# Performance work log

Measured on AMD Instinct MI355X. Metric: run time of the kernel, lower is better.

## Reference

```python
import jax, jax.numpy as jnp
import numpy as np

D_MODEL = 1024
NUM_EXPERTS = 16
TOP_K = 2
TOP_C = 4  # min(M, max(4, 2*K))
RANK = 64  # max(4, d_model // 16) per choose_lowrank_r
TAU = 1.0


def setup_inputs() -> dict:
    key = jax.random.key(0)
    ks = jax.random.split(key, 7)
    B = 32768
    x = jax.random.normal(ks[0], (B, D_MODEL), dtype=jnp.float32)
    # shared encoder Linear(d, d) with bias
    We = jax.random.normal(ks[1], (D_MODEL, D_MODEL), dtype=jnp.float32) / np.sqrt(D_MODEL)
    be = jnp.zeros((D_MODEL,), dtype=jnp.float32)
    # gating Linear(d, M), no bias
    Wg = jax.random.normal(ks[2], (NUM_EXPERTS, D_MODEL), dtype=jnp.float32) / np.sqrt(D_MODEL)
    # per-expert LoRA weights: U: [M, r, d], V: [M, d, r], gamma: [M]
    U = jax.random.normal(ks[3], (NUM_EXPERTS, RANK, D_MODEL), dtype=jnp.float32) / np.sqrt(D_MODEL)
    V = jax.random.normal(ks[4], (NUM_EXPERTS, D_MODEL, RANK), dtype=jnp.float32) / np.sqrt(RANK)
    gamma = jnp.ones((NUM_EXPERTS,), dtype=jnp.float32)
    return {"x": x, "We": We, "be": be, "Wg": Wg, "U": U, "V": V, "gamma": gamma}


def reference(x, We, be, Wg, U, V, gamma):
    B = x.shape[0]
    encoded = x @ We.T + be                       # [B, d]
    logits = (encoded @ Wg.T) / TAU               # [B, M]
    # Top-C candidate selection, then Top-K among candidates
    topc_vals, topc_idx = jax.lax.top_k(logits, TOP_C)          # [B, C]
    topk_vals, pos_in_c = jax.lax.top_k(topc_vals, TOP_K)       # [B, K]
    topk_idx = jnp.take_along_axis(topc_idx, pos_in_c, axis=1)  # [B, K]
    # masked stable softmax over selected logits (matches _stable_masked_softmax)
    e = jnp.exp(topk_vals - jnp.max(topk_vals, axis=1, keepdims=True))
    w = e / (jnp.sum(e, axis=1, keepdims=True) + 1e-12)
    w = jnp.where(w > 1e-12, w, 0.0)  # keep_mask: drop negligible weights
    # scatter routing weights into dense [B, M] combine matrix
    w_full = jnp.zeros((B, NUM_EXPERTS), x.dtype).at[
        jnp.arange(B)[:, None], topk_idx].add(w)
    # expert residual delta: E(x) = x + gamma * V @ silu(U @ x)
    hidden = jax.nn.silu(jnp.einsum('bd,mrd->bmr', encoded, U))  # [B, M, r]
    delta = jnp.einsum('bmr,mdr,bm->bd', hidden, V, w_full * gamma[None, :])
    # y = encoded + sum_k w_k * (E_k(encoded) - encoded); sum_k w_k = 1
    return encoded + delta
```

## Files before the change

### kernel.cpp

```cpp
#include <hip/hip_runtime.h>
#include <stdint.h>

#define B_TOK 32768
#define DM 1024
#define NEXP 16
#define RK 64
#define NPAIR 256
#define TPT 64
#define HT 128
#define GRID_CMB 3072
#define GRID_HID 544
#define MAXTILE 1024

typedef unsigned short u16;
typedef __bf16 bf16x8 __attribute__((ext_vector_type(8)));
typedef float f32x4 __attribute__((ext_vector_type(4)));

__device__ __forceinline__ u16 f2bf(float f) {
  union { float f; uint32_t u; } v; v.f = f;
  return (u16)((v.u + 0x7fffu + ((v.u >> 16) & 1u)) >> 16);
}
__device__ __forceinline__ float bf2f(u16 u) {
  union { uint32_t i; float f; } v; v.i = ((uint32_t)u) << 16; return v.f;
}

__device__ __forceinline__ void gload_lds16(const void* g, void* l) {
  __builtin_amdgcn_global_load_lds(
      (const __attribute__((address_space(1))) void*)g,
      (__attribute__((address_space(3))) void*)l, 16, 0, 0);
}

__global__ void k_convert(const float* __restrict__ src, u16* __restrict__ dst, int n4) {
  int i = blockIdx.x * blockDim.x + threadIdx.x;
  int stride = gridDim.x * blockDim.x;
  for (; i < n4; i += stride) {
    float4 v = reinterpret_cast<const float4*>(src)[i];
    ushort4 o;
    o.x = f2bf(v.x); o.y = f2bf(v.y); o.z = f2bf(v.z); o.w = f2bf(v.w);
    reinterpret_cast<ushort4*>(dst)[i] = o;
  }
}

__global__ void k_wgeff(const float* __restrict__ Wg, const float* __restrict__ We,
                        const float* __restrict__ be,
                        float* __restrict__ Wgeff, float* __restrict__ gbias) {
  int e = blockIdx.y;
  int d = blockIdx.x * 256 + threadIdx.x;
  double acc = 0.0;
  for (int k = 0; k < DM; ++k)
    acc += (double)Wg[e * DM + k] * (double)We[k * DM + d];
  Wgeff[e * DM + d] = (float)acc;
  if (blockIdx.x == 0 && threadIdx.x == 0) {
    double s = 0.0;
    for (int k = 0; k < DM; ++k) s += (double)be[k] * (double)Wg[e * DM + k];
    gbias[e] = (float)s;
  }
}

#define GT 64
#define GD 128

__global__ __launch_bounds__(256) void k_gating(
    const float* __restrict__ x, u16* __restrict__ x_bf,
    const float* __restrict__ Wgeff, const float* __restrict__ gbias,
    const float* __restrict__ gamma,
    int* __restrict__ tk_pid, float* __restrict__ tk_w0, float* __restrict__ tk_w1,
    int* __restrict__ counts_p, int* __restrict__ counts_e) {
  __shared__ float xs[GT][GD + 4];
  __shared__ float wsd[NEXP][GD + 4];
  __shared__ float lg[GT][NEXP + 2];
  __shared__ int bcnt[NPAIR];
  __shared__ int bexp[NEXP];
  const int tid = threadIdx.x;
  const int tok0 = blockIdx.x * GT;
  const int t0 = (tid >> 3) * 2;
  const int e0 = (tid & 7) * 2;
  bcnt[tid] = 0;
  if (tid < NEXP) bexp[tid] = 0;

  double acc00 = 0.0, acc01 = 0.0, acc10 = 0.0, acc11 = 0.0;

  for (int c = 0; c < DM; c += GD) {
    __syncthreads();
    #pragma unroll
    for (int v = 0; v < (GT * GD / 4) / 256; ++v) {
      int idx = tid + v * 256;
      int r = idx >> 5, cc = idx & 31;
      float4 v4 = *reinterpret_cast<const float4*>(x + (size_t)(tok0 + r) * DM + c + cc * 4);
      *reinterpret_cast<float4*>(&xs[r][cc * 4]) = v4;
      ushort4 o;
      o.x = f2bf(v4.x); o.y = f2bf(v4.y); o.z = f2bf(v4.z); o.w = f2bf(v4.w);
      *reinterpret_cast<ushort4*>(x_bf + (size_t)(tok0 + r) * DM + c + cc * 4) = o;
    }
    #pragma unroll
    for (int v = 0; v < (NEXP * GD / 4) / 256; ++v) {
      int idx = tid + v * 256;
      int r = idx >> 5, cc = idx & 31;
      *reinterpret_cast<float4*>(&wsd[r][cc * 4]) =
          *reinterpret_cast<const float4*>(Wgeff + (size_t)r * DM + c + cc * 4);
    }
    __syncthreads();
    #pragma unroll 8
    for (int d = 0; d < GD; d += 4) {
      float4 xa = *reinterpret_cast<const float4*>(&xs[t0][d]);
      float4 xb = *reinterpret_cast<const float4*>(&xs[t0 + 1][d]);
      float4 wa = *reinterpret_cast<const float4*>(&wsd[e0][d]);
      float4 wb = *reinterpret_cast<const float4*>(&wsd[e0 + 1][d]);
      acc00 += (double)xa.x * wa.x + (double)xa.y * wa.y + (double)xa.z * wa.z + (double)xa.w * wa.w;
      acc01 += (double)xa.x * wb.x + (double)xa.y * wb.y + (double)xa.z * wb.z + (double)xa.w * wb.w;
      acc10 += (double)xb.x * wa.x + (double)xb.y * wa.y + (double)xb.z * wa.z + (double)xb.w * wa.w;
      acc11 += (double)xb.x * wb.x + (double)xb.y * wb.y + (double)xb.z * wb.z + (double)xb.w * wb.w;
    }
  }

  lg[t0][e0]         = (float)(acc00 + (double)gbias[e0]);
  lg[t0][e0 + 1]     = (float)(acc01 + (double)gbias[e0 + 1]);
  lg[t0 + 1][e0]     = (float)(acc10 + (double)gbias[e0]);
  lg[t0 + 1][e0 + 1] = (float)(acc11 + (double)gbias[e0 + 1]);
  __syncthreads();

  if (tid < GT) {
    int tok = tok0 + tid;
    float v0 = lg[tid][0]; int i0 = 0;
    #pragma unroll
    for (int j = 1; j < NEXP; ++j)
      if (lg[tid][j] > v0) { v0 = lg[tid][j]; i0 = j; }
    float v1 = -3.4e38f; int i1 = 0;
    #pragma unroll
    for (int j = 0; j < NEXP; ++j) {
      if (j == i0) continue;
      if (lg[tid][j] > v1) { v1 = lg[tid][j]; i1 = j; }
    }
    float e1 = expf(v1 - v0);
    float denom = 1.0f + e1 + 1e-12f;
    float w0 = 1.0f / denom, w1 = e1 / denom;
    if (!(w0 > 1e-12f)) w0 = 0.0f;
    if (!(w1 > 1e-12f)) w1 = 0.0f;
    int pid = i0 * 16 + i1;
    tk_pid[tok] = pid;
    tk_w0[tok] = w0 * gamma[i0];
    tk_w1[tok] = w1 * gamma[i1];
    atomicAdd(&bcnt[pid], 1);
    atomicAdd(&bexp[i0], 1);
    atomicAdd(&bexp[i1], 1);
  }
  __syncthreads();
  if (bcnt[tid] > 0) atomicAdd(&counts_p[tid], bcnt[tid]);
  if (tid < NEXP && bexp[tid] > 0) atomicAdd(&counts_e[tid], bexp[tid]);
}

__global__ __launch_bounds__(NPAIR) void k_scan(
    const int* __restrict__ counts_p, const int* __restrict__ counts_e,
    int* __restrict__ offs_p, int* __restrict__ curs_p,
    int* __restrict__ offs_e, int* __restrict__ curs_e,
    int* __restrict__ tp_pair, int* __restrict__ tp_loc, int* __restrict__ n_tp,
    int* __restrict__ th_exp, int* __restrict__ th_loc, int* __restrict__ n_th) {
  __shared__ int sc[NPAIR], st[NPAIR];
  __shared__ int seb[NEXP + 1], thb[NEXP + 1];
  const int tid = threadIdx.x;
  const int c = counts_p[tid];
  const int nt = (c + TPT - 1) / TPT;
  sc[tid] = c; st[tid] = nt;
  __syncthreads();
  for (int s = 1; s < NPAIR; s <<= 1) {
    int vc = 0, vt = 0;
    if (tid >= s) { vc = sc[tid - s]; vt = st[tid - s]; }
    __syncthreads();
    sc[tid] += vc; st[tid] += vt;
    __syncthreads();
  }
  const int offc = sc[tid] - c;
  const int offt = st[tid] - nt;
  offs_p[tid] = offc;
  curs_p[tid] = offc;
  if (tid == NPAIR - 1) { offs_p[NPAIR] = sc[tid]; n_tp[0] = st[tid]; }
  for (int q = 0; q < nt; ++q) { tp_pair[offt + q] = tid; tp_loc[offt + q] = q * TPT; }

  if (tid == 0) {
    int s = 0, s2 = 0;
    for (int e = 0; e < NEXP; ++e) {
      seb[e] = s; thb[e] = s2;
      int ce = counts_e[e];
      s += ce; s2 += (ce + HT - 1) / HT;
    }
    seb[NEXP] = s; thb[NEXP] = s2;
    n_th[0] = s2;
  }
  __syncthreads();
  if (tid <= NEXP) offs_e[tid] = seb[tid];
  if (tid < NEXP) {
    curs_e[tid] = seb[tid];
    int ce = counts_e[tid];
    int ntt = (ce + HT - 1) / HT;
    for (int q = 0; q < ntt; ++q) { th_exp[thb[tid] + q] = tid; th_loc[thb[tid] + q] = q * HT; }
  }
}

__global__ __launch_bounds__(256) void k_scatter(
    const int* __restrict__ tk_pid, const float* __restrict__ tk_w0,
    const float* __restrict__ tk_w1,
    int* __restrict__ curs_p, int* __restrict__ curs_e,
    int* __restrict__ a_tok, int* __restrict__ a_h0,
    int* __restrict__ a_h1,
    int* __restrict__ e_tok, float* __restrict__ e_w) {
  __shared__ int hp[NPAIR];
  __shared__ int he[NEXP];
  __shared__ int bp[NPAIR];
  __shared__ int beB[NEXP];
  const int tid = threadIdx.x;
  const int tok = blockIdx.x * 256 + tid;
  hp[tid] = 0;
  if (tid < NEXP) he[tid] = 0;
  __syncthreads();

  const int pid = tk_pid[tok];
  const int i0 = pid >> 4, i1 = pid & 15;
  const int rp = atomicAdd(&hp[pid], 1);
  const int r0 = atomicAdd(&he[i0], 1);
  const int r1 = atomicAdd(&he[i1], 1);
  __syncthreads();

  if (hp[tid] > 0) bp[tid] = atomicAdd(&curs_p[tid], hp[tid]);
  if (tid < NEXP && he[tid] > 0) beB[tid] = atomicAdd(&curs_e[tid], he[tid]);
  __syncthreads();

  const int posp = bp[pid] + rp;
  const int pos0 = beB[i0] + r0;
  const int pos1 = beB[i1] + r1;
  a_tok[posp] = tok;
  a_h0[posp] = pos0;
  a_h1[posp] = pos1;
  e_tok[pos0] = tok; e_w[pos0] = tk_w0[tok];
  e_tok[pos1] = tok; e_w[pos1] = tk_w1[tok];
}

__global__ __launch_bounds__(256) void k_encoder(
    const u16* __restrict__ A, const u16* __restrict__ Bm,
    const float* __restrict__ bias, u16* __restrict__ Cb) {
  __shared__ __align__(16) u16 As[128 * 32];
  __shared__ __align__(16) u16 Bs[128 * 32];
  const int nwg = gridDim.x * gridDim.y;
  const int orig = blockIdx.y * gridDim.x + blockIdx.x;
  const int qq = nwg >> 3;
  const int swz = (orig & 7) * qq + (orig >> 3);
  const int m0 = (swz / gridDim.x) * 128, n0 = (swz % gridDim.x) * 128;
  const int tid = threadIdx.x;
  const int lane = tid & 63, wave = tid >> 6;
  const int wr = wave >> 1, wc = wave & 1;

  f32x4 acc[4][4];
  #pragma unroll
  for (int i = 0; i < 4; ++i)
    #pragma unroll
    for (int j = 0; j < 4; ++j) acc[i][j] = (f32x4){0.f, 0.f, 0.f, 0.f};

  const int srow = tid >> 2;
  const int scol = (tid & 3) * 8;
  const int lrow = lane & 15, lk = (lane >> 4) * 8;

  const u16* ga1 = A + (size_t)(m0 + srow) * DM + scol;
  const u16* ga2 = A + (size_t)(m0 + 64 + srow) * DM + scol;
  const u16* gb1 = Bm + (size_t)(n0 + srow) * DM + scol;
  const u16* gb2 = Bm + (size_t)(n0 + 64 + srow) * DM + scol;

  for (int k0 = 0; k0 < DM; k0 += 32) {
    __syncthreads();
    gload_lds16(ga1 + k0, As + srow * 32 + scol);
    gload_lds16(ga2 + k0, As + (64 + srow) * 32 + scol);
    gload_lds16(gb1 + k0, Bs + srow * 32 + scol);
    gload_lds16(gb2 + k0, Bs + (64 + srow) * 32 + scol);
    __syncthreads();
    bf16x8 a[4], b[4];
    #pragma unroll
    for (int mi = 0; mi < 4; ++mi)
      a[mi] = *reinterpret_cast<const bf16x8*>(&As[(wr * 64 + mi * 16 + lrow) * 32 + lk]);
    #pragma unroll
    for (int nj = 0; nj < 4; ++nj)
      b[nj] = *reinterpret_cast<const bf16x8*>(&Bs[(wc * 64 + nj * 16 + lrow) * 32 + lk]);
    #pragma unroll
    for (int mi = 0; mi < 4; ++mi)
      #pragma unroll
      for (int nj = 0; nj < 4; ++nj)
        acc[mi][nj] = __builtin_amdgcn_mfma_f32_16x16x32_bf16(a[mi], b[nj], acc[mi][nj], 0, 0, 0);
  }

  const int orow = (lane >> 4) * 4, ocol = lane & 15;
  #pragma unroll
  for (int mi = 0; mi < 4; ++mi) {
    #pragma unroll
    for (int nj = 0; nj < 4; ++nj) {
      int gcol = n0 + wc * 64 + nj * 16 + ocol;
      float bv = bias[gcol];
      #pragma unroll
      for (int r = 0; r < 4; ++r) {
        int grow = m0 + wr * 64 + mi * 16 + orow + r;
        Cb[(size_t)grow * DM + gcol] = f2bf(acc[mi][nj][r] + bv);
      }
    }
  }
}

__global__ __launch_bounds__(256) void k_hidden(
    const u16* __restrict__ Enc, const u16* __restrict__ Ub,
    const int* __restrict__ offs_e, const int* __restrict__ th_exp,
    const int* __restrict__ th_loc, const int* __restrict__ n_th,
    const int* __restrict__ e_tok, const float* __restrict__ e_w,
    u16* __restrict__ Hws) {
  const int bswz = (blockIdx.x & 7) * (GRID_HID >> 3) + (blockIdx.x >> 3);
  if (bswz >= n_th[0]) return;
  const int e = th_exp[bswz];
  const int loc0 = th_loc[bswz];
  const int base = offs_e[e];
  const int cnt = offs_e[e + 1] - base;
  const int tid = threadIdx.x;
  const int lane = tid & 63, wave = tid >> 6;
  const int lrow = lane & 15;
  const int lkb = (lane >> 4) * 16;

  __shared__ float s_ew[HT];
  __shared__ __align__(16) u16 Us[64 * 512];
  if (tid < HT) {
    int i = loc0 + tid;
    s_ew[tid] = (i < cnt) ? e_w[base + i] : 0.0f;
  }

  const u16* aP[2];
  #pragma unroll
  for (int mi = 0; mi < 2; ++mi) {
    int ridx = loc0 + wave * 32 + mi * 16 + lrow;
    int v = ridx < cnt;
    int tok = e_tok[base + (v ? ridx : 0)];
    aP[mi] = Enc + (size_t)tok * DM + (lane >> 4) * 8;
  }

  f32x4 acc[2][4];
  #pragma unroll
  for (int i = 0; i < 2; ++i)
    #pragma unroll
    for (int j = 0; j < 4; ++j) acc[i][j] = (f32x4){0.f, 0.f, 0.f, 0.f};

  const char* Ue = (const char*)(Ub + (size_t)e * RK * DM);

  for (int half = 0; half < 2; ++half) {
    __syncthreads();
    #pragma unroll
    for (int it = 0; it < 16; ++it) {
      int D = (tid + it * 256) * 16;
      int row = D >> 10, bo = D & 1023;
      int sbo = bo ^ ((row & 7) << 4);
      gload_lds16(Ue + (size_t)row * 2048 + half * 1024 + sbo, ((char*)Us) + D);
    }
    __syncthreads();
    #pragma unroll 4
    for (int step = 0; step < 16; ++step) {
      const int k0 = half * 512 + step * 32;
      bf16x8 b[4];
      #pragma unroll
      for (int nj = 0; nj < 4; ++nj) {
        int n = nj * 16 + lrow;
        int bofs = n * 1024 + ((step * 64 + lkb) ^ ((n & 7) << 4));
        b[nj] = *reinterpret_cast<const bf16x8*>(((const char*)Us) + bofs);
      }
      bf16x8 a0 = *reinterpret_cast<const bf16x8*>(aP[0] + k0);
      bf16x8 a1 = *reinterpret_cast<const bf16x8*>(aP[1] + k0);
      #pragma unroll
      for (int nj = 0; nj < 4; ++nj) {
        acc[0][nj] = __builtin_amdgcn_mfma_f32_16x16x32_bf16(a0, b[nj], acc[0][nj], 0, 0, 0);
        acc[1][nj] = __builtin_amdgcn_mfma_f32_16x16x32_bf16(a1, b[nj], acc[1][nj], 0, 0, 0);
      }
    }
  }

  #pragma unroll
  for (int mi = 0; mi < 2; ++mi)
    #pragma unroll
    for (int nj = 0; nj < 4; ++nj)
      #pragma unroll
      for (int rr = 0; rr < 4; ++rr) {
        int rloc = wave * 32 + mi * 16 + (lane >> 4) * 4 + rr;
        if (loc0 + rloc < cnt) {
          float z = acc[mi][nj][rr];
          float h = z / (1.0f + expf(-z)) * s_ew[rloc];
          Hws[(size_t)(base + loc0 + rloc) * RK + nj * 16 + (lane & 15)] = f2bf(h);
        }
      }
}

__global__ __launch_bounds__(256) void k_combine(
    const u16* __restrict__ Enc, const u16* __restrict__ Vb,
    const u16* __restrict__ Hws, const int* __restrict__ offs_p,
    const int* __restrict__ tp_pair, const int* __restrict__ tp_loc,
    const int* __restrict__ n_tp, const int* __restrict__ a_tok,
    const int* __restrict__ a_h0, const int* __restrict__ a_h1,
    float* __restrict__ Out) {
  const int bswz = (blockIdx.x & 7) * (GRID_CMB >> 3) + (blockIdx.x >> 3);
  const int t = bswz >> 2;
  const int p = bswz & 3;
  if (t >= n_tp[0]) return;
  const int pid = tp_pair[t];
  const int pe0 = pid >> 4, pe1 = pid & 15;
  const int base = offs_p[pid];
  const int cnt = offs_p[pid + 1] - base;
  const int loc0 = tp_loc[t];
  const int tid = threadIdx.x;
  const int lane = tid & 63, wave = tid >> 6;

  __shared__ int s_tok[TPT];
  __shared__ int s_h0[TPT];
  __shared__ int s_h1[TPT];
  __shared__ int s_val[TPT];
  if (tid < TPT) {
    int idx = loc0 + tid;
    int v = idx < cnt;
    int pp = base + (v ? idx : 0);
    s_val[tid] = v;
    s_tok[tid] = a_tok[pp];
    s_h0[tid] = a_h0[pp];
    s_h1[tid] = a_h1[pp];
  }
  __syncthreads();

  const int lrow = lane & 15, lk = (lane >> 4) * 8;

  bf16x8 hb[4][4];
  #pragma unroll
  for (int kk = 0; kk < 4; ++kk)
    #pragma unroll
    for (int tf = 0; tf < 4; ++tf) {
      int tok = tf * 16 + lrow;
      int hidx = (kk < 2) ? s_h0[tok] : s_h1[tok];
      hb[kk][tf] = *reinterpret_cast<const bf16x8*>(
          Hws + (size_t)hidx * RK + (kk & 1) * 32 + lk);
    }

  const u16* V0 = Vb + (size_t)pe0 * DM * RK;
  const u16* V1 = Vb + (size_t)pe1 * DM * RK;

  const int col0 = p * 256 + wave * 64;
  f32x4 acc2[4][4];
  #pragma unroll
  for (int i = 0; i < 4; ++i)
    #pragma unroll
    for (int j = 0; j < 4; ++j) acc2[i][j] = (f32x4){0.f, 0.f, 0.f, 0.f};

  #pragma unroll
  for (int kk = 0; kk < 4; ++kk) {
    const u16* Vsel = (kk < 2) ? V0 : V1;
    const int kof = (kk & 1) * 32 + lk;
    #pragma unroll
    for (int mi = 0; mi < 4; ++mi) {
      int d = col0 + mi * 16 + lrow;
      bf16x8 va = *reinterpret_cast<const bf16x8*>(Vsel + (size_t)d * RK + kof);
      #pragma unroll
      for (int tf = 0; tf < 4; ++tf)
        acc2[mi][tf] = __builtin_amdgcn_mfma_f32_16x16x32_bf16(va, hb[kk][tf], acc2[mi][tf], 0, 0, 0);
    }
  }

  #pragma unroll
  for (int mi = 0; mi < 4; ++mi)
    #pragma unroll
    for (int tf = 0; tf < 4; ++tf) {
      int tok = tf * 16 + (lane & 15);
      if (!s_val[tok]) continue;
      int d = col0 + mi * 16 + (lane >> 4) * 4;
      size_t ro = (size_t)s_tok[tok] * DM + d;
      ushort4 ev = *reinterpret_cast<const ushort4*>(Enc + ro);
      float4 o;
      o.x = acc2[mi][tf][0] + bf2f(ev.x);
      o.y = acc2[mi][tf][1] + bf2f(ev.y);
      o.z = acc2[mi][tf][2] + bf2f(ev.z);
      o.w = acc2[mi][tf][3] + bf2f(ev.w);
      *reinterpret_cast<float4*>(Out + ro) = o;
    }
}

extern "C" void kernel_launch(void* const* d_in, const int* in_sizes, int n_in,
                              void* d_out, int out_size, void* d_ws, size_t ws_size,
                              hipStream_t stream) {
  const float* x = (const float*)d_in[0];
  const float* We = (const float*)d_in[1];
  const float* be = (const float*)d_in[2];
  const float* Wg = (const float*)d_in[3];
  const float* U = (const float*)d_in[4];
  const float* V = (const float*)d_in[5];
  const float* gamma = (const float*)d_in[6];
  float* Out = (float*)d_out;

  char* ws = (char*)d_ws;
  size_t off = 0;
  auto alloc = [&](size_t bytes) -> void* {
    void* p = ws + off;
    off += (bytes + 255) & ~(size_t)255;
    return p;
  };
  u16* x_bf   = (u16*)alloc((size_t)B_TOK * DM * 2);
  u16* enc_bf = (u16*)alloc((size_t)B_TOK * DM * 2);
  u16* We_bf  = (u16*)alloc((size_t)DM * DM * 2);
  u16* U_bf   = (u16*)alloc((size_t)NEXP * RK * DM * 2);
  u16* V_bf   = (u16*)alloc((size_t)NEXP * DM * RK * 2);
  u16* Hws    = (u16*)alloc(((size_t)2 * B_TOK + HT) * RK * 2);
  float* Wgeff = (float*)alloc((size_t)NEXP * DM * 4);
  float* gbias = (float*)alloc(NEXP * 4);
  int* tk_pid  = (int*)alloc((size_t)B_TOK * 4);
  float* tk_w0 = (float*)alloc((size_t)B_TOK * 4);
  float* tk_w1 = (float*)alloc((size_t)B_TOK * 4);
  int* counts_p = (int*)alloc(NPAIR * 4);
  int* counts_e = (int*)alloc(NEXP * 4);
  int* offs_p   = (int*)alloc((NPAIR + 1) * 4);
  int* curs_p   = (int*)alloc(NPAIR * 4);
  int* offs_e   = (int*)alloc((NEXP + 1) * 4);
  int* curs_e   = (int*)alloc(NEXP * 4);
  int* tp_pair  = (int*)alloc(MAXTILE * 4);
  int* tp_loc   = (int*)alloc(MAXTILE * 4);
  int* n_tp     = (int*)alloc(256);
  int* th_exp   = (int*)alloc(MAXTILE * 4);
  int* th_loc   = (int*)alloc(MAXTILE * 4);
  int* n_th     = (int*)alloc(256);
  int* a_tok   = (int*)alloc((size_t)B_TOK * 4);
  int* a_h0    = (int*)alloc((size_t)B_TOK * 4);
  int* a_h1    = (int*)alloc((size_t)B_TOK * 4);
  int* e_tok   = (int*)alloc(((size_t)2 * B_TOK + HT) * 4);
  float* e_w   = (float*)alloc(((size_t)2 * B_TOK + HT) * 4);
  (void)ws_size; (void)in_sizes; (void)n_in; (void)out_size;

  hipMemsetAsync(counts_p, 0, NPAIR * 4, stream);
  hipMemsetAsync(counts_e, 0, NEXP * 4, stream);

  k_convert<<<256, 256, 0, stream>>>(We, We_bf, DM * DM / 4);
  k_convert<<<256, 256, 0, stream>>>(U, U_bf, NEXP * RK * DM / 4);
  k_convert<<<256, 256, 0, stream>>>(V, V_bf, NEXP * DM * RK / 4);
  k_wgeff<<<dim3(4, 16), 256, 0, stream>>>(Wg, We, be, Wgeff, gbias);
  k_gating<<<B_TOK / GT, 256, 0, stream>>>(x, x_bf, Wgeff, gbias, gamma,
                                           tk_pid, tk_w0, tk_w1, counts_p, counts_e);
  k_scan<<<1, NPAIR, 0, stream>>>(counts_p, counts_e, offs_p, curs_p, offs_e, curs_e,
                                  tp_pair, tp_loc, n_tp, th_exp, th_loc, n_th);
  k_scatter<<<B_TOK / 256, 256, 0, stream>>>(tk_pid, tk_w0, tk_w1, curs_p, curs_e,
                                             a_tok, a_h0, a_h1, e_tok, e_w);
  k_encoder<<<dim3(DM / 128, B_TOK / 128), 256, 0, stream>>>(x_bf, We_bf, be, enc_bf);
  k_hidden<<<GRID_HID, 256, 0, stream>>>(enc_bf, U_bf, offs_e, th_exp, th_loc, n_th,
                                         e_tok, e_w, Hws);
  k_combine<<<GRID_CMB, 256, 0, stream>>>(enc_bf, V_bf, Hws, offs_p, tp_pair, tp_loc,
                                          n_tp, a_tok, a_h0, a_h1, Out);
}
```

Measured before the change: 392.6 us.

## Widen encoder K-tile with XOR-swizzled LDS, stage epilogue, prefetch residual loads

The encoder GEMM now loads 64-wide K slices into LDS using an XOR swizzle to avoid bank conflicts, which halves the number of sync barriers per K loop. Its epilogue writes results to shared memory first and then stores them with coalesced 16-byte global writes instead of scattered 2-byte stores. In the combine kernel, the encoded residual values are loaded before the MFMA loop so their latency overlaps with the compute. These changes add register pressure from the prefetched residuals, and the shared-memory footprint grows to 32KB.

```diff
diff --git a/kernel.cpp b/kernel.cpp
--- a/kernel.cpp
+++ b/kernel.cpp
@@ -237,8 +237,9 @@
 __global__ __launch_bounds__(256) void k_encoder(
     const u16* __restrict__ A, const u16* __restrict__ Bm,
     const float* __restrict__ bias, u16* __restrict__ Cb) {
-  __shared__ __align__(16) u16 As[128 * 32];
-  __shared__ __align__(16) u16 Bs[128 * 32];
+  __shared__ __align__(16) u16 SM[128 * 128];
+  u16* As = SM;
+  u16* Bs = SM + 128 * 64;
   const int nwg = gridDim.x * gridDim.y;
   const int orig = blockIdx.y * gridDim.x + blockIdx.x;
   const int qq = nwg >> 3;
@@ -247,6 +248,7 @@
   const int tid = threadIdx.x;
   const int lane = tid & 63, wave = tid >> 6;
   const int wr = wave >> 1, wc = wave & 1;
+  const int lrow = lane & 15, lhi = lane >> 4;
 
   f32x4 acc[4][4];
   #pragma unroll
@@ -254,50 +256,61 @@
     #pragma unroll
     for (int j = 0; j < 4; ++j) acc[i][j] = (f32x4){0.f, 0.f, 0.f, 0.f};
 
-  const int srow = tid >> 2;
-  const int scol = (tid & 3) * 8;
-  const int lrow = lane & 15, lk = (lane >> 4) * 8;
-
-  const u16* ga1 = A + (size_t)(m0 + srow) * DM + scol;
-  const u16* ga2 = A + (size_t)(m0 + 64 + srow) * DM + scol;
-  const u16* gb1 = Bm + (size_t)(n0 + srow) * DM + scol;
-  const u16* gb2 = Bm + (size_t)(n0 + 64 + srow) * DM + scol;
-
-  for (int k0 = 0; k0 < DM; k0 += 32) {
-    __syncthreads();
-    gload_lds16(ga1 + k0, As + srow * 32 + scol);
-    gload_lds16(ga2 + k0, As + (64 + srow) * 32 + scol);
-    gload_lds16(gb1 + k0, Bs + srow * 32 + scol);
-    gload_lds16(gb2 + k0, Bs + (64 + srow) * 32 + scol);
-    __syncthreads();
-    bf16x8 a[4], b[4];
+  for (int k0 = 0; k0 < DM; k0 += 64) {
+    __syncthreads();
+    #pragma unroll
+    for (int j = 0; j < 4; ++j) {
+      int slot = wave * 256 + j * 64 + lane;
+      int r = slot >> 3, c = slot & 7;
+      int sc = (c ^ (r & 7)) << 3;
+      gload_lds16(A + (size_t)(m0 + r) * DM + k0 + sc, As + slot * 8);
+      gload_lds16(Bm + (size_t)(n0 + r) * DM + k0 + sc, Bs + slot * 8);
+    }
+    __syncthreads();
+    #pragma unroll
+    for (int kk = 0; kk < 2; ++kk) {
+      bf16x8 a[4], b[4];
+      #pragma unroll
+      for (int mi = 0; mi < 4; ++mi) {
+        int r = wr * 64 + mi * 16 + lrow;
+        a[mi] = *reinterpret_cast<const bf16x8*>(
+            As + r * 64 + ((((kk << 2) + lhi) ^ (r & 7)) << 3));
+      }
+      #pragma unroll
+      for (int nj = 0; nj < 4; ++nj) {
+        int r = wc * 64 + nj * 16 + lrow;
+        b[nj] = *reinterpret_cast<const bf16x8*>(
+            Bs + r * 64 + ((((kk << 2) + lhi) ^ (r & 7)) << 3));
+      }
+      #pragma unroll
+      for (int mi = 0; mi < 4; ++mi)
+        #pragma unroll
+        for (int nj = 0; nj < 4; ++nj)
+          acc[mi][nj] = __builtin_amdgcn_mfma_f32_16x16x32_bf16(a[mi], b[nj], acc[mi][nj], 0, 0, 0);
+    }
+  }
+
+  __syncthreads();
+  const int orow = lhi * 4, ocol = lrow;
+  #pragma unroll
+  for (int nj = 0; nj < 4; ++nj) {
+    int col_l = wc * 64 + nj * 16 + ocol;
+    float bv = bias[n0 + col_l];
     #pragma unroll
     for (int mi = 0; mi < 4; ++mi)
-      a[mi] = *reinterpret_cast<const bf16x8*>(&As[(wr * 64 + mi * 16 + lrow) * 32 + lk]);
-    #pragma unroll
-    for (int nj = 0; nj < 4; ++nj)
-      b[nj] = *reinterpret_cast<const bf16x8*>(&Bs[(wc * 64 + nj * 16 + lrow) * 32 + lk]);
-    #pragma unroll
-    for (int mi = 0; mi < 4; ++mi)
-      #pragma unroll
-      for (int nj = 0; nj < 4; ++nj)
-        acc[mi][nj] = __builtin_amdgcn_mfma_f32_16x16x32_bf16(a[mi], b[nj], acc[mi][nj], 0, 0, 0);
-  }
-
-  const int orow = (lane >> 4) * 4, ocol = lane & 15;
-  #pragma unroll
-  for (int mi = 0; mi < 4; ++mi) {
-    #pragma unroll
-    for (int nj = 0; nj < 4; ++nj) {
-      int gcol = n0 + wc * 64 + nj * 16 + ocol;
-      float bv = bias[gcol];
       #pragma unroll
       for (int r = 0; r < 4; ++r) {
-        int grow = m0 + wr * 64 + mi * 16 + orow + r;
-        Cb[(size_t)grow * DM + gcol] = f2bf(acc[mi][nj][r] + bv);
+        int row_l = wr * 64 + mi * 16 + orow + r;
+        SM[row_l * 128 + col_l] = f2bf(acc[mi][nj][r] + bv);
       }
-    }
-  }
+  }
+  __syncthreads();
+  const int row_o = tid >> 1;
+  const int off = (tid & 1) * 64;
+  #pragma unroll
+  for (int v = 0; v < 8; ++v)
+    *reinterpret_cast<uint4*>(Cb + (size_t)(m0 + row_o) * DM + n0 + off + v * 8) =
+        *reinterpret_cast<const uint4*>(SM + row_o * 128 + off + v * 8);
 }
 
 __global__ __launch_bounds__(256) void k_hidden(
@@ -421,6 +434,7 @@
   __syncthreads();
 
   const int lrow = lane & 15, lk = (lane >> 4) * 8;
+  const int col0 = p * 256 + wave * 64;
 
   bf16x8 hb[4][4];
   #pragma unroll
@@ -433,10 +447,19 @@
           Hws + (size_t)hidx * RK + (kk & 1) * 32 + lk);
     }
 
+  ushort4 encv[4][4];
+  #pragma unroll
+  for (int mi = 0; mi < 4; ++mi)
+    #pragma unroll
+    for (int tf = 0; tf < 4; ++tf) {
+      int tok = tf * 16 + (lane & 15);
+      int d = col0 + mi * 16 + (lane >> 4) * 4;
+      encv[mi][tf] = *reinterpret_cast<const ushort4*>(Enc + (size_t)s_tok[tok] * DM + d);
+    }
+
   const u16* V0 = Vb + (size_t)pe0 * DM * RK;
   const u16* V1 = Vb + (size_t)pe1 * DM * RK;
 
-  const int col0 = p * 256 + wave * 64;
   f32x4 acc2[4][4];
   #pragma unroll
   for (int i = 0; i < 4; ++i)
@@ -465,7 +488,7 @@
       if (!s_val[tok]) continue;
       int d = col0 + mi * 16 + (lane >> 4) * 4;
       size_t ro = (size_t)s_tok[tok] * DM + d;
-      ushort4 ev = *reinterpret_cast<const ushort4*>(Enc + ro);
+      ushort4 ev = encv[mi][tf];
       float4 o;
       o.x = acc2[mi][tf][0] + bf2f(ev.x);
       o.y = acc2[mi][tf][1] + bf2f(ev.y);
```

New measurement: 392.7 us. No clear change (+0.0%).
